# Performance work log

Hardware: AMD Instinct MI355X
Metric: run time of the kernel (lower is better)

## Reference

```python
import jax, jax.numpy as jnp
import numpy as np

B, S, HID = 2, 2048, 2048
H, HKV, HD = 16, 8, 128
INPUT_CHUNK, RET_CHUNK = 256, 64
NUM_CHUNKS = S // INPUT_CHUNK - 1          # 7 retrieval chunks
INPUT_START = NUM_CHUNKS * RET_CHUNK       # 448
KV_LEN = S + INPUT_START                   # 2496
SCALE = HD ** -0.5


def _document_id():
    d = np.zeros(KV_LEN, np.int32)
    d[INPUT_START:] = -1
    for i in range(NUM_CHUNKS):            # retrieval chunks get ids 1..NUM_CHUNKS
        d[RET_CHUNK * i: RET_CHUNK * (i + 1)] = i + 1
    for i in range(1, NUM_CHUNKS + 1):     # input chunk i (i>=1) gets id i
        d[INPUT_START + INPUT_CHUNK * i: INPUT_START + INPUT_CHUNK * (i + 1)] = i
    return d


def _causal_retrieval_mask():
    d = _document_id()
    q = np.arange(S)[:, None]
    kv = np.arange(KV_LEN)[None, :]
    causal = (q + INPUT_START >= kv) & (kv > INPUT_START)
    docm = (d[q + INPUT_START] == d[kv]) & (kv < INPUT_START)
    return jnp.asarray(causal | docm)      # [S, KV_LEN] bool


_MASK = _causal_retrieval_mask()


def rotate_half(x):
    x1, x2 = jnp.split(x, 2, axis=-1)
    return jnp.concatenate([-x2, x1], axis=-1)


def setup_inputs() -> dict:
    key = jax.random.key(0)
    ks = jax.random.split(key, 8)
    hidden_states = jax.random.normal(ks[0], (B, S, HID), jnp.float32)
    # standard llama RoPE tables
    pos = jnp.arange(S, dtype=jnp.float32)
    inv = 1.0 / (10000.0 ** (jnp.arange(0, HD, 2, dtype=jnp.float32) / HD))
    f = pos[:, None] * inv[None, :]
    emb = jnp.concatenate([f, f], axis=-1)
    cos = jnp.broadcast_to(jnp.cos(emb), (B, S, HD)).astype(jnp.float32)
    sin = jnp.broadcast_to(jnp.sin(emb), (B, S, HD)).astype(jnp.float32)
    retrieval_key_states = jax.random.normal(ks[1], (B * NUM_CHUNKS, HKV, RET_CHUNK, HD), jnp.float32)
    retrieval_value_states = jax.random.normal(ks[2], (B * NUM_CHUNKS, HKV, RET_CHUNK, HD), jnp.float32)
    s = 0.02
    Wq = jax.random.normal(ks[3], (HID, H * HD), jnp.float32) * s
    Wk = jax.random.normal(ks[4], (HID, HKV * HD), jnp.float32) * s
    Wv = jax.random.normal(ks[5], (HID, HKV * HD), jnp.float32) * s
    Wo = jax.random.normal(ks[6], (H * HD, HID), jnp.float32) * s
    return {"hidden_states": hidden_states, "cos": cos, "sin": sin,
            "retrieval_key_states": retrieval_key_states,
            "retrieval_value_states": retrieval_value_states,
            "Wq": Wq, "Wk": Wk, "Wv": Wv, "Wo": Wo}


def reference(hidden_states, cos, sin, retrieval_key_states, retrieval_value_states, Wq, Wk, Wv, Wo):
    b = hidden_states.shape[0]
    # QKV projections (bias=False), -> [b, h, s, d]
    q = (hidden_states @ Wq).reshape(b, S, H, HD).transpose(0, 2, 1, 3)
    k = (hidden_states @ Wk).reshape(b, S, HKV, HD).transpose(0, 2, 1, 3)
    v = (hidden_states @ Wv).reshape(b, S, HKV, HD).transpose(0, 2, 1, 3)
    # RoPE (cos/sin unsqueezed over heads)
    c = cos[:, None]
    sn = sin[:, None]
    q = q * c + rotate_half(q) * sn
    k = k * c + rotate_half(k) * sn
    # retrieval KV: (b*nc, hkv, rc, d) -> (b, hkv, nc*rc, d)
    rk = retrieval_key_states.reshape(b, NUM_CHUNKS, HKV, RET_CHUNK, HD).transpose(0, 2, 1, 3, 4).reshape(b, HKV, NUM_CHUNKS * RET_CHUNK, HD)
    rv = retrieval_value_states.reshape(b, NUM_CHUNKS, HKV, RET_CHUNK, HD).transpose(0, 2, 1, 3, 4).reshape(b, HKV, NUM_CHUNKS * RET_CHUNK, HD)
    k_all = jnp.concatenate([rk, k], axis=2)     # [b, hkv, KV_LEN, d]
    v_all = jnp.concatenate([rv, v], axis=2)
    # GQA: repeat kv heads
    g = H // HKV
    k_all = jnp.repeat(k_all, g, axis=1)
    v_all = jnp.repeat(v_all, g, axis=1)
    scores = jnp.einsum('bhqd,bhkd->bhqk', q, k_all) * SCALE
    neg = jnp.finfo(scores.dtype).min
    scores = jnp.where(_MASK[None, None], scores, neg)
    probs = jax.nn.softmax(scores, axis=-1)
    # fully-masked rows (q_idx=0) -> 0 output, matching flex_attention semantics
    probs = jnp.where(_MASK[None, None], probs, 0.0)
    attn = jnp.einsum('bhqk,bhkd->bhqd', probs, v_all)   # [b, H, S, HD]
    # NOTE: source reshapes (b, H, S, HD) directly to (b, S, H*HD) with NO transpose
    attn = attn.reshape(b, S, H * HD)
    return attn @ Wo
```

## Files before the change

### kernel.cpp

```cpp
#include <hip/hip_runtime.h>

#define B_ 2
#define S_ 2048
#define HID_ 2048
#define H_ 16
#define HKV_ 8
#define HD_ 128
#define NCH_ 7
#define RET_ 64
#define IST_ 448
#define KVL_ 2496
#define SCALE_ 0.08838834764831845f
#define SC2_ (0.08838834764831845f * 1.44269504088896340f)
#define MCAP_ 16.0f

typedef __attribute__((ext_vector_type(8))) short short8;
typedef __attribute__((ext_vector_type(4))) float f32x4;

static __device__ __forceinline__ unsigned short f2bf(float f) {
    unsigned u = __float_as_uint(f);
    unsigned r = (u + 0x7fffu + ((u >> 16) & 1u)) >> 16;
    return (unsigned short)r;
}
static __device__ __forceinline__ float bf2f(unsigned short x) {
    return __uint_as_float(((unsigned)x) << 16);
}

#define GLL16(gp, lp) __builtin_amdgcn_global_load_lds( \
    (__attribute__((address_space(1))) void*)(void*)(gp), \
    (__attribute__((address_space(3))) void*)(void*)(lp), 16, 0, 0)

__global__ __launch_bounds__(256) void cvt_f32_bf16(const float* __restrict__ x,
                                                    unsigned short* __restrict__ y, int n4) {
    int i = blockIdx.x * 256 + threadIdx.x;
    if (i >= n4) return;
    float4 v = ((const float4*)x)[i];
    ushort4 o;
    o.x = f2bf(v.x); o.y = f2bf(v.y); o.z = f2bf(v.z); o.w = f2bf(v.w);
    ((ushort4*)y)[i] = o;
}

__global__ void transpose_all(const float* __restrict__ Wq, const float* __restrict__ Wk,
                              const float* __restrict__ Wv, const float* __restrict__ Wo,
                              unsigned short* __restrict__ wqkvT, unsigned short* __restrict__ woT) {
    __shared__ float t[32][33];
    const int z = blockIdx.z;
    const float* W;
    unsigned short* WT;
    int N;
    if (z == 0)      { W = Wq; WT = wqkvT;                        N = 2048; }
    else if (z == 1) { W = Wk; WT = wqkvT + (size_t)2048 * 2048;  N = 1024; }
    else if (z == 2) { W = Wv; WT = wqkvT + (size_t)3072 * 2048;  N = 1024; }
    else             { W = Wo; WT = woT;                          N = 2048; }
    const int k0 = blockIdx.x << 5, n0 = blockIdx.y << 5;
    if (n0 >= N) return;
    const int tx = threadIdx.x, ty = threadIdx.y;
#pragma unroll
    for (int i = 0; i < 4; i++)
        t[ty + i * 8][tx] = W[(size_t)(k0 + ty + i * 8) * N + n0 + tx];
    __syncthreads();
#pragma unroll
    for (int i = 0; i < 4; i++)
        WT[(size_t)(n0 + ty + i * 8) * 2048 + k0 + tx] = f2bf(t[tx][ty + i * 8]);
}

template <int BN, typename OT>
__global__ __launch_bounds__(512, 2) void gemm256(const unsigned short* __restrict__ A,
                                                  const unsigned short* __restrict__ BT,
                                                  OT* __restrict__ C,
                                                  int M, int N, int K) {
    constexpr int NJ = BN / 64;
    __shared__ short As[2][16384];
    __shared__ short Bs[2][BN * 64];
    const int tid = threadIdx.x;
    const int wid = tid >> 6, lane = tid & 63;
    const int lq = lane & 15, lk = lane >> 4;
    const int wm = wid >> 2, wn = wid & 3;
    const int bm = blockIdx.x, bn = blockIdx.y;

    const int rowin = tid >> 3;
    const int koff = (((tid & 7) ^ (rowin & 7)) << 3);
    const size_t abase = (size_t)(bm * 256 + rowin) * K;
    const size_t bbase = (size_t)(bn * BN + rowin) * K;
    const int ldst = wid * 512;

    f32x4 acc[8][NJ] = {};

    auto stage = [&](int buf, int k0) {
#pragma unroll
        for (int r = 0; r < 4; r++)
            GLL16(A + abase + (size_t)(r * 64) * K + k0 + koff, &As[buf][r * 4096 + ldst]);
#pragma unroll
        for (int r = 0; r < NJ; r++)
            GLL16(BT + bbase + (size_t)(r * 64) * K + k0 + koff, &Bs[buf][r * 4096 + ldst]);
    };

    const int nk = K >> 6;
    stage(0, 0);
    __syncthreads();
    for (int t = 0; t < nk; t++) {
        const int cur = t & 1;
        if (t + 1 < nk) stage(cur ^ 1, (t + 1) << 6);
        short8 bf[2][NJ];
#pragma unroll
        for (int j = 0; j < NJ; j++)
#pragma unroll
            for (int kk = 0; kk < 2; kk++) {
                const int row = wn * (BN / 4) + j * 16 + lq;
                bf[kk][j] = *(const short8*)&Bs[cur][row * 64 +
                                                     (((kk * 4 + lk) ^ (lq & 7)) << 3)];
            }
#pragma unroll
        for (int p = 0; p < 4; p++) {
            short8 af0[2], af1[2];
#pragma unroll
            for (int kk = 0; kk < 2; kk++) {
                const int r0 = wm * 128 + (2 * p) * 16 + lq;
                const int r1 = wm * 128 + (2 * p + 1) * 16 + lq;
                af0[kk] = *(const short8*)&As[cur][r0 * 64 +
                                                   (((kk * 4 + lk) ^ (lq & 7)) << 3)];
                af1[kk] = *(const short8*)&As[cur][r1 * 64 +
                                                   (((kk * 4 + lk) ^ (lq & 7)) << 3)];
            }
            __builtin_amdgcn_s_setprio(1);
#pragma unroll
            for (int j = 0; j < NJ; j++)
#pragma unroll
                for (int kk = 0; kk < 2; kk++) {
                    acc[2 * p][j] =
                        __builtin_amdgcn_mfma_f32_16x16x32_bf16(bf[kk][j], af0[kk], acc[2 * p][j], 0, 0, 0);
                    acc[2 * p + 1][j] =
                        __builtin_amdgcn_mfma_f32_16x16x32_bf16(bf[kk][j], af1[kk], acc[2 * p + 1][j], 0, 0, 0);
                }
            __builtin_amdgcn_s_setprio(0);
        }
        __syncthreads();
    }
#pragma unroll
    for (int i = 0; i < 8; i++) {
        const size_t row = (size_t)(bm * 256 + wm * 128 + i * 16 + lq);
#pragma unroll
        for (int j = 0; j < NJ; j++) {
            const size_t col = (size_t)(bn * BN + wn * (BN / 4) + j * 16 + lk * 4);
            if constexpr (sizeof(OT) == 2) {
                ushort4 u;
                u.x = f2bf(acc[i][j][0]);
                u.y = f2bf(acc[i][j][1]);
                u.z = f2bf(acc[i][j][2]);
                u.w = f2bf(acc[i][j][3]);
                *(ushort4*)&C[row * N + col] = u;
            } else {
                *(f32x4*)&C[row * N + col] = acc[i][j];
            }
        }
    }
}

__global__ __launch_bounds__(256) void prep_k_kernel(const unsigned short* __restrict__ qkvraw,
                                                     const float* __restrict__ cosb,
                                                     const float* __restrict__ sinb,
                                                     const float* __restrict__ rk,
                                                     unsigned short* __restrict__ kall) {
    const int bid = blockIdx.x;
    if (bid < 8192) {
        size_t idx = (size_t)bid * 256 + threadIdx.x;
        int d = idx & 63;
        int hk = (idx >> 6) & 7;
        size_t bs = idx >> 9;
        size_t base = bs * 4096 + 2048 + hk * 128 + d;
        int b = (int)(bs >> 11), s = (int)(bs & 2047);
        float x1 = bf2f(qkvraw[base]), x2 = bf2f(qkvraw[base + 64]);
        float c1 = cosb[(size_t)s * 128 + d], sn1 = sinb[(size_t)s * 128 + d];
        float c2 = cosb[(size_t)s * 128 + d + 64], sn2 = sinb[(size_t)s * 128 + d + 64];
        size_t o = ((size_t)(b * HKV_ + hk) * KVL_ + IST_ + s) * HD_ + d;
        kall[o] = f2bf(x1 * c1 - x2 * sn1);
        kall[o + 64] = f2bf(x2 * c2 + x1 * sn2);
    } else {
        size_t idx = (size_t)(bid - 8192) * 256 + threadIdx.x;
        int d = idx & 127;
        int r = (idx >> 7) & 63;
        int hk = (idx >> 13) & 7;
        int bc = (int)(idx >> 16);
        int b = bc / NCH_, ch = bc % NCH_;
        kall[((size_t)(b * HKV_ + hk) * KVL_ + ch * RET_ + r) * HD_ + d] = f2bf(rk[idx]);
    }
}

__global__ void prep_v_kernel(const unsigned short* __restrict__ qkvraw,
                              const float* __restrict__ rv,
                              unsigned short* __restrict__ vt) {
    const int bid = blockIdx.x;
    const int tx = threadIdx.x, ty = threadIdx.y;
    if (bid < 4096) {
        __shared__ unsigned short t[32][33];
        const int d0 = (bid & 3) << 5, s0 = ((bid >> 2) & 63) << 5;
        const int bh = bid >> 8;
        const int b = bh >> 3, hk = bh & 7;
#pragma unroll
        for (int i = 0; i < 4; i++)
            t[ty + i * 8][tx] =
                qkvraw[(size_t)(b * S_ + s0 + ty + i * 8) * 4096 + 3072 + hk * 128 + d0 + tx];
        __syncthreads();
#pragma unroll
        for (int i = 0; i < 4; i++)
            vt[((size_t)(b * HKV_ + hk) * HD_ + d0 + ty + i * 8) * KVL_ + IST_ + s0 + tx] =
                t[tx][ty + i * 8];
    } else {
        __shared__ float tf[32][33];
        const int bid2 = bid - 4096;
        const int d0 = (bid2 & 3) << 5;
        const int r0 = ((bid2 >> 2) & 1) << 5;
        const int z = bid2 >> 3;
        const int bc = z >> 3, hk = z & 7;
        const int b = bc / NCH_, ch = bc % NCH_;
#pragma unroll
        for (int i = 0; i < 4; i++)
            tf[ty + i * 8][tx] =
                rv[((size_t)(bc * HKV_ + hk) * RET_ + r0 + ty + i * 8) * HD_ + d0 + tx];
        __syncthreads();
#pragma unroll
        for (int i = 0; i < 4; i++)
            vt[((size_t)(b * HKV_ + hk) * HD_ + d0 + ty + i * 8) * KVL_ + ch * RET_ + r0 + tx] =
                f2bf(tf[tx][ty + i * 8]);
    }
}

__global__ __launch_bounds__(1024) void attn_kernel(const unsigned short* __restrict__ qkvraw,
                                                    const unsigned short* __restrict__ kall,
                                                    const unsigned short* __restrict__ vt,
                                                    const float* __restrict__ cosb,
                                                    const float* __restrict__ sinb,
                                                    unsigned short* __restrict__ attnb) {
    __shared__ short Ks[2][16384];
    __shared__ short Vs[2][16384];
    __shared__ short Ps[16][1024];
    const int tid = threadIdx.x;
    const int wid = tid >> 6, lane = tid & 63;
    const int lq = lane & 15, lk = lane >> 4;
    const int pairi = blockIdx.x;
    const int h = blockIdx.y, b = blockIdx.z, hk = h >> 1;
    const unsigned short* kbase = kall + (size_t)(b * HKV_ + hk) * KVL_ * HD_;
    const unsigned short* vbase = vt + (size_t)(b * HKV_ + hk) * HD_ * KVL_;

    int row_[2], xc_[2];
#pragma unroll
    for (int p = 0; p < 2; p++) {
        int o = p * 16384 + tid * 16;
        row_[p] = o >> 8;
        xc_[p] = (tid & 15) ^ (row_[p] & 7);
    }
    short* psw = &Ps[wid][0];

    const int qlo = pairi * 128, qhi = (15 - pairi) * 128;
    const int wgrp = wid >> 3;
    const int qb0 = wgrp ? qhi : qlo;
    const int qbw = qb0 + (wid & 7) * 16;
    const int doc_lo = qlo >> 8;
    const int doc_hi = qhi >> 8;
    const int kvA = RET_ * ((doc_lo >= 1 ? doc_lo : 1) - 1);
    const int kvB = RET_ * (doc_hi - 1);
    const int nt = 17 - pairi;

    const unsigned short* qrp = qkvraw + ((size_t)(b * S_) + qbw + lq) * 4096 + h * 128;
    short8 qr[4];
#pragma unroll
    for (int d = 0; d < 4; d++) qr[d] = *(const short8*)(qrp + d * 32 + lk * 8);
    const float* cosp = cosb + (size_t)(qbw + lq) * 128 + lk * 8;
    const float* sinp = sinb + (size_t)(qbw + lq) * 128 + lk * 8;
    short8 qf[4];
#pragma unroll
    for (int d = 0; d < 4; d++) {
        float4 c0 = *(const float4*)(cosp + d * 32);
        float4 c1 = *(const float4*)(cosp + d * 32 + 4);
        float4 s0 = *(const float4*)(sinp + d * 32);
        float4 s1 = *(const float4*)(sinp + d * 32 + 4);
        const float cc[8] = {c0.x, c0.y, c0.z, c0.w, c1.x, c1.y, c1.z, c1.w};
        const float ss[8] = {s0.x, s0.y, s0.z, s0.w, s1.x, s1.y, s1.z, s1.w};
        const int od = d ^ 2;
        const float sg = (d < 2) ? -1.f : 1.f;
#pragma unroll
        for (int e = 0; e < 8; e++) {
            float x = bf2f((unsigned short)qr[d][e]);
            float y = bf2f((unsigned short)qr[od][e]);
            qf[d][e] = (short)f2bf(fmaf(sg * y, ss[e], x * cc[e]));
        }
    }

    f32x4 o[8] = {};
    float lsump = 0.f;

    auto stage = [&](int buf, int kv0) {
#pragma unroll
        for (int p = 0; p < 2; p++) {
            GLL16(kbase + (size_t)(kv0 + row_[p]) * HD_ + xc_[p] * 8,
                  &Ks[buf][p * 8192 + wid * 512]);
            GLL16(vbase + (size_t)row_[p] * KVL_ + kv0 + xc_[p] * 8,
                  &Vs[buf][p * 8192 + wid * 512]);
        }
    };
    auto stage_ret = [&](int buf) {
#pragma unroll
        for (int p = 0; p < 2; p++) {
            int kr = row_[p];
            int ks = (kr < 64) ? kvA + kr : kvB + (kr - 64);
            GLL16(kbase + (size_t)ks * HD_ + xc_[p] * 8, &Ks[buf][p * 8192 + wid * 512]);
            int vc = (xc_[p] < 8) ? kvA + xc_[p] * 8 : kvB + (xc_[p] - 8) * 8;
            GLL16(vbase + (size_t)row_[p] * KVL_ + vc, &Vs[buf][p * 8192 + wid * 512]);
        }
    };
    auto smpv = [&](f32x4* sa4, int hb8, const char* vb) {
#pragma unroll
        for (int j2 = 0; j2 < 4; j2++) {
            float p0 = __builtin_amdgcn_exp2f(fmaf(sa4[j2][0], SC2_, -MCAP_));
            float p1 = __builtin_amdgcn_exp2f(fmaf(sa4[j2][1], SC2_, -MCAP_));
            float p2 = __builtin_amdgcn_exp2f(fmaf(sa4[j2][2], SC2_, -MCAP_));
            float p3 = __builtin_amdgcn_exp2f(fmaf(sa4[j2][3], SC2_, -MCAP_));
            lsump += (p0 + p1) + (p2 + p3);
            uint2 w;
            w.x = ((unsigned)f2bf(p1) << 16) | f2bf(p0);
            w.y = ((unsigned)f2bf(p3) << 16) | f2bf(p2);
            *(uint2*)((char*)psw + (lq * 128 + ((j2 * 32 + lk * 8) ^ ((lq & 7) << 4)))) = w;
        }
        __builtin_amdgcn_s_setprio(1);
#pragma unroll
        for (int ks = 0; ks < 2; ks++) {
            short8 pa = *(const short8*)((const char*)psw +
                                         (lq * 128 + (((ks * 4 + lk) ^ (lq & 7)) << 4)));
#pragma unroll
            for (int db = 0; db < 8; db++) {
                short8 vf = *(const short8*)(vb + ((db * 16 + lq) * 256 +
                                                   (((hb8 + ks * 4 + lk) ^ (lq & 7)) << 4)));
                o[db] = __builtin_amdgcn_mfma_f32_16x16x32_bf16(pa, vf, o[db], 0, 0, 0);
            }
        }
        __builtin_amdgcn_s_setprio(0);
    };

    stage_ret(0);
    asm volatile("s_waitcnt vmcnt(0)" ::: "memory");
    __syncthreads();
    int cur = 0;
    for (int t = 0; t < nt; t++) {
        if (t + 1 < nt) stage(cur ^ 1, IST_ + t * 128);
        const char* kb = (const char*)&Ks[cur][0];
        const char* vb = (const char*)&Vs[cur][0];
        if (t == 0) {
            const bool retact = (wgrp == 1) || (doc_lo >= 1);
            if (retact) {
                const int hh = wgrp;
                f32x4 sa[4] = {};
                __builtin_amdgcn_s_setprio(1);
#pragma unroll
                for (int d = 0; d < 4; d++)
#pragma unroll
                    for (int j2 = 0; j2 < 4; j2++) {
                        short8 kf = *(const short8*)(kb + (((hh * 4 + j2) * 16 + lq) * 256 +
                                                           (((d * 4 + lk) ^ (lq & 7)) << 4)));
                        sa[j2] = __builtin_amdgcn_mfma_f32_16x16x32_bf16(kf, qf[d], sa[j2], 0, 0, 0);
                    }
                __builtin_amdgcn_s_setprio(0);
                smpv(sa, hh * 8, vb);
            }
        } else {
            const int kv0 = IST_ + (t - 1) * 128;
            const bool active = kv0 <= qbw + 15 + IST_;
            if (active) {
                f32x4 sa[8] = {};
                __builtin_amdgcn_s_setprio(1);
#pragma unroll
                for (int d = 0; d < 4; d++)
#pragma unroll
                    for (int j = 0; j < 8; j++) {
                        short8 kf = *(const short8*)(kb + ((j * 16 + lq) * 256 +
                                                           (((d * 4 + lk) ^ (lq & 7)) << 4)));
                        sa[j] = __builtin_amdgcn_mfma_f32_16x16x32_bf16(kf, qf[d], sa[j], 0, 0, 0);
                    }
                __builtin_amdgcn_s_setprio(0);
                const bool needMask = (kv0 == IST_) || (kv0 + 127 > qbw + IST_);
                if (needMask) {
                    const int qg = qbw + lq;
#pragma unroll
                    for (int j = 0; j < 8; j++)
#pragma unroll
                        for (int r = 0; r < 4; r++) {
                            int kg = kv0 + j * 16 + lk * 4 + r;
                            if (!(kg > IST_ && kg <= qg + IST_)) sa[j][r] = -3e38f;
                        }
                }
                smpv(&sa[0], 0, vb);
                smpv(&sa[4], 8, vb);
            }
        }
        if (t + 1 < nt) asm volatile("s_waitcnt vmcnt(0)" ::: "memory");
        __syncthreads();
        cur ^= 1;
    }

    float ls = lsump;
    ls += __shfl_xor(ls, 16);
    ls += __shfl_xor(ls, 32);
    float inv[4];
#pragma unroll
    for (int r = 0; r < 4; r++) {
        float v = __shfl(ls, lk * 4 + r);
        inv[r] = v > 0.f ? 1.f / v : 0.f;
    }
#pragma unroll
    for (int db = 0; db < 8; db++)
#pragma unroll
        for (int r = 0; r < 4; r++) {
            int qg = qbw + lk * 4 + r;
            size_t row = (size_t)b * 2048 + h * 128 + (qg >> 4);
            size_t col = (size_t)(qg & 15) * 128 + db * 16 + lq;
            attnb[row * 2048 + col] = f2bf(o[db][r] * inv[r]);
        }
}

extern "C" void kernel_launch(void* const* d_in, const int* in_sizes, int n_in,
                              void* d_out, int out_size, void* d_ws, size_t ws_size,
                              hipStream_t stream) {
    const float* hidden = (const float*)d_in[0];
    const float* cosb = (const float*)d_in[1];
    const float* sinb = (const float*)d_in[2];
    const float* rk = (const float*)d_in[3];
    const float* rv = (const float*)d_in[4];
    const float* Wq = (const float*)d_in[5];
    const float* Wk = (const float*)d_in[6];
    const float* Wv = (const float*)d_in[7];
    const float* Wo = (const float*)d_in[8];
    float* out = (float*)d_out;

    char* ws = (char*)d_ws;
    unsigned short* hb     = (unsigned short*)(ws + 0);
    unsigned short* wqkvT  = (unsigned short*)(ws + 16777216);
    unsigned short* woT    = (unsigned short*)(ws + 33554432);
    unsigned short* qkvraw = (unsigned short*)(ws + 41943040);
    unsigned short* kallb  = (unsigned short*)(ws + 92274688);
    unsigned short* vtb    = (unsigned short*)(ws + 102498304);
    unsigned short* attnb  = (unsigned short*)(ws + 112721920);

    cvt_f32_bf16<<<8192, 256, 0, stream>>>(hidden, hb, 2097152);
    transpose_all<<<dim3(64, 64, 4), dim3(32, 8), 0, stream>>>(Wq, Wk, Wv, Wo, wqkvT, woT);

    gemm256<256, unsigned short><<<dim3(16, 16), 512, 0, stream>>>(hb, wqkvT, qkvraw, 4096, 4096, 2048);

    prep_k_kernel<<<11776, 256, 0, stream>>>(qkvraw, cosb, sinb, rk, kallb);
    prep_v_kernel<<<4992, dim3(32, 8), 0, stream>>>(qkvraw, rv, vtb);

    attn_kernel<<<dim3(8, 16, 2), 1024, 0, stream>>>(qkvraw, kallb, vtb, cosb, sinb, attnb);

    gemm256<128, float><<<dim3(16, 16), 512, 0, stream>>>(attnb, woT, out, 4096, 2048, 2048);
}
```

Measured before the change: 221.8 us.

## Merge K/V prep kernels, use packed bf16 convert, skip masked half-tiles

Combines the K and V preparation kernels into one launch, removing a launch gap. Replaces the manual float-to-bf16 rounding in the softmax P path with the hardware v_cvt_pk_bf16_f32 instruction. In causal attention tiles, the second 64-column half of the QK and PV MFMAs is skipped when it lies entirely above the diagonal for the warp's rows. This adds some branching and relies on the hardware conversion rounding the same way as the software version.

```diff
diff --git a/kernel.cpp b/kernel.cpp
--- a/kernel.cpp
+++ b/kernel.cpp
@@ -156,14 +156,17 @@
     }
 }
 
-__global__ __launch_bounds__(256) void prep_k_kernel(const unsigned short* __restrict__ qkvraw,
-                                                     const float* __restrict__ cosb,
-                                                     const float* __restrict__ sinb,
-                                                     const float* __restrict__ rk,
-                                                     unsigned short* __restrict__ kall) {
+__global__ __launch_bounds__(256) void prep_kv_kernel(const unsigned short* __restrict__ qkvraw,
+                                                      const float* __restrict__ cosb,
+                                                      const float* __restrict__ sinb,
+                                                      const float* __restrict__ rk,
+                                                      const float* __restrict__ rv,
+                                                      unsigned short* __restrict__ kall,
+                                                      unsigned short* __restrict__ vt) {
     const int bid = blockIdx.x;
+    const int tid = threadIdx.x;
     if (bid < 8192) {
-        size_t idx = (size_t)bid * 256 + threadIdx.x;
+        size_t idx = (size_t)bid * 256 + tid;
         int d = idx & 63;
         int hk = (idx >> 6) & 7;
         size_t bs = idx >> 9;
@@ -175,53 +178,49 @@
         size_t o = ((size_t)(b * HKV_ + hk) * KVL_ + IST_ + s) * HD_ + d;
         kall[o] = f2bf(x1 * c1 - x2 * sn1);
         kall[o + 64] = f2bf(x2 * c2 + x1 * sn2);
-    } else {
-        size_t idx = (size_t)(bid - 8192) * 256 + threadIdx.x;
+    } else if (bid < 11776) {
+        size_t idx = (size_t)(bid - 8192) * 256 + tid;
         int d = idx & 127;
         int r = (idx >> 7) & 63;
         int hk = (idx >> 13) & 7;
         int bc = (int)(idx >> 16);
         int b = bc / NCH_, ch = bc % NCH_;
         kall[((size_t)(b * HKV_ + hk) * KVL_ + ch * RET_ + r) * HD_ + d] = f2bf(rk[idx]);
-    }
-}
-
-__global__ void prep_v_kernel(const unsigned short* __restrict__ qkvraw,
-                              const float* __restrict__ rv,
-                              unsigned short* __restrict__ vt) {
-    const int bid = blockIdx.x;
-    const int tx = threadIdx.x, ty = threadIdx.y;
-    if (bid < 4096) {
-        __shared__ unsigned short t[32][33];
-        const int d0 = (bid & 3) << 5, s0 = ((bid >> 2) & 63) << 5;
-        const int bh = bid >> 8;
-        const int b = bh >> 3, hk = bh & 7;
-#pragma unroll
-        for (int i = 0; i < 4; i++)
-            t[ty + i * 8][tx] =
-                qkvraw[(size_t)(b * S_ + s0 + ty + i * 8) * 4096 + 3072 + hk * 128 + d0 + tx];
-        __syncthreads();
-#pragma unroll
-        for (int i = 0; i < 4; i++)
-            vt[((size_t)(b * HKV_ + hk) * HD_ + d0 + ty + i * 8) * KVL_ + IST_ + s0 + tx] =
-                t[tx][ty + i * 8];
     } else {
-        __shared__ float tf[32][33];
-        const int bid2 = bid - 4096;
-        const int d0 = (bid2 & 3) << 5;
-        const int r0 = ((bid2 >> 2) & 1) << 5;
-        const int z = bid2 >> 3;
-        const int bc = z >> 3, hk = z & 7;
-        const int b = bc / NCH_, ch = bc % NCH_;
-#pragma unroll
-        for (int i = 0; i < 4; i++)
-            tf[ty + i * 8][tx] =
-                rv[((size_t)(bc * HKV_ + hk) * RET_ + r0 + ty + i * 8) * HD_ + d0 + tx];
-        __syncthreads();
-#pragma unroll
-        for (int i = 0; i < 4; i++)
-            vt[((size_t)(b * HKV_ + hk) * HD_ + d0 + ty + i * 8) * KVL_ + ch * RET_ + r0 + tx] =
-                f2bf(tf[tx][ty + i * 8]);
+        const int vbid = bid - 11776;
+        const int tx = tid & 31, ty = tid >> 5;
+        if (vbid < 4096) {
+            __shared__ unsigned short t[32][33];
+            const int d0 = (vbid & 3) << 5, s0 = ((vbid >> 2) & 63) << 5;
+            const int bh = vbid >> 8;
+            const int b = bh >> 3, hk = bh & 7;
+#pragma unroll
+            for (int i = 0; i < 4; i++)
+                t[ty + i * 8][tx] =
+                    qkvraw[(size_t)(b * S_ + s0 + ty + i * 8) * 4096 + 3072 + hk * 128 + d0 + tx];
+            __syncthreads();
+#pragma unroll
+            for (int i = 0; i < 4; i++)
+                vt[((size_t)(b * HKV_ + hk) * HD_ + d0 + ty + i * 8) * KVL_ + IST_ + s0 + tx] =
+                    t[tx][ty + i * 8];
+        } else {
+            __shared__ float tf[32][33];
+            const int bid2 = vbid - 4096;
+            const int d0 = (bid2 & 3) << 5;
+            const int r0 = ((bid2 >> 2) & 1) << 5;
+            const int z = bid2 >> 3;
+            const int bc = z >> 3, hk = z & 7;
+            const int b = bc / NCH_, ch = bc % NCH_;
+#pragma unroll
+            for (int i = 0; i < 4; i++)
+                tf[ty + i * 8][tx] =
+                    rv[((size_t)(bc * HKV_ + hk) * RET_ + r0 + ty + i * 8) * HD_ + d0 + tx];
+            __syncthreads();
+#pragma unroll
+            for (int i = 0; i < 4; i++)
+                vt[((size_t)(b * HKV_ + hk) * HD_ + d0 + ty + i * 8) * KVL_ + ch * RET_ + r0 + tx] =
+                    f2bf(tf[tx][ty + i * 8]);
+        }
     }
 }
 
@@ -317,8 +316,8 @@
             float p3 = __builtin_amdgcn_exp2f(fmaf(sa4[j2][3], SC2_, -MCAP_));
             lsump += (p0 + p1) + (p2 + p3);
             uint2 w;
-            w.x = ((unsigned)f2bf(p1) << 16) | f2bf(p0);
-            w.y = ((unsigned)f2bf(p3) << 16) | f2bf(p2);
+            asm("v_cvt_pk_bf16_f32 %0, %1, %2" : "=v"(w.x) : "v"(p0), "v"(p1));
+            asm("v_cvt_pk_bf16_f32 %0, %1, %2" : "=v"(w.y) : "v"(p2), "v"(p3));
             *(uint2*)((char*)psw + (lq * 128 + ((j2 * 32 + lk * 8) ^ ((lq & 7) << 4)))) = w;
         }
         __builtin_amdgcn_s_setprio(1);
@@ -365,30 +364,49 @@
             const int kv0 = IST_ + (t - 1) * 128;
             const bool active = kv0 <= qbw + 15 + IST_;
             if (active) {
+                const bool act2 = (kv0 + 64 <= qbw + 15 + IST_);
                 f32x4 sa[8] = {};
                 __builtin_amdgcn_s_setprio(1);
 #pragma unroll
                 for (int d = 0; d < 4; d++)
 #pragma unroll
-                    for (int j = 0; j < 8; j++) {
+                    for (int j = 0; j < 4; j++) {
                         short8 kf = *(const short8*)(kb + ((j * 16 + lq) * 256 +
                                                            (((d * 4 + lk) ^ (lq & 7)) << 4)));
                         sa[j] = __builtin_amdgcn_mfma_f32_16x16x32_bf16(kf, qf[d], sa[j], 0, 0, 0);
                     }
+                if (act2) {
+#pragma unroll
+                    for (int d = 0; d < 4; d++)
+#pragma unroll
+                        for (int j = 4; j < 8; j++) {
+                            short8 kf = *(const short8*)(kb + ((j * 16 + lq) * 256 +
+                                                               (((d * 4 + lk) ^ (lq & 7)) << 4)));
+                            sa[j] = __builtin_amdgcn_mfma_f32_16x16x32_bf16(kf, qf[d], sa[j], 0, 0, 0);
+                        }
+                }
                 __builtin_amdgcn_s_setprio(0);
-                const bool needMask = (kv0 == IST_) || (kv0 + 127 > qbw + IST_);
-                if (needMask) {
-                    const int qg = qbw + lq;
-#pragma unroll
-                    for (int j = 0; j < 8; j++)
+                const int qg = qbw + lq;
+                if (kv0 == IST_ || kv0 + 63 > qbw + IST_) {
+#pragma unroll
+                    for (int j = 0; j < 4; j++)
 #pragma unroll
                         for (int r = 0; r < 4; r++) {
                             int kg = kv0 + j * 16 + lk * 4 + r;
                             if (!(kg > IST_ && kg <= qg + IST_)) sa[j][r] = -3e38f;
                         }
                 }
+                if (act2 && kv0 + 127 > qbw + IST_) {
+#pragma unroll
+                    for (int j = 4; j < 8; j++)
+#pragma unroll
+                        for (int r = 0; r < 4; r++) {
+                            int kg = kv0 + j * 16 + lk * 4 + r;
+                            if (kg > qg + IST_) sa[j][r] = -3e38f;
+                        }
+                }
                 smpv(&sa[0], 0, vb);
-                smpv(&sa[4], 8, vb);
+                if (act2) smpv(&sa[4], 8, vb);
             }
         }
         if (t + 1 < nt) asm volatile("s_waitcnt vmcnt(0)" ::: "memory");
@@ -444,8 +462,7 @@
 
     gemm256<256, unsigned short><<<dim3(16, 16), 512, 0, stream>>>(hb, wqkvT, qkvraw, 4096, 4096, 2048);
 
-    prep_k_kernel<<<11776, 256, 0, stream>>>(qkvraw, cosb, sinb, rk, kallb);
-    prep_v_kernel<<<4992, dim3(32, 8), 0, stream>>>(qkvraw, rv, vtb);
+    prep_kv_kernel<<<16768, 256, 0, stream>>>(qkvraw, cosb, sinb, rk, rv, kallb, vtb);
 
     attn_kernel<<<dim3(8, 16, 2), 1024, 0, stream>>>(qkvraw, kallb, vtb, cosb, sinb, attnb);
 
```

After: 220.8 us. Within noise of the previous version (-0.4%).
